# Performance work log

Hardware: AMD Instinct MI355X
Metric: run time of the kernel (lower is better)

Reference implementation:

```python
import jax, jax.numpy as jnp
import numpy as np

H = 16      # num_attention_heads
D = 1024    # hidden_size
HD = D // H # head dim = 64
ALPHA = 0.5


def setup_inputs() -> dict:
    key = jax.random.key(0)
    ks = jax.random.split(key, 12)
    B, S = 4, 1024
    s = 0.02
    return {
        "hidden_states": jax.random.normal(ks[0], (B, S, D), jnp.float32),
        "attention_mask": jnp.zeros((B, 1, 1, S), jnp.float32),
        "previous_attention": jax.random.uniform(ks[1], (B, H, S, S), jnp.float32),
        "Wq": jax.random.normal(ks[2], (D, D), jnp.float32) * s,
        "bq": jnp.zeros((D,), jnp.float32),
        "Wk": jax.random.normal(ks[3], (D, D), jnp.float32) * s,
        "bk": jnp.zeros((D,), jnp.float32),
        "Wv": jax.random.normal(ks[4], (D, D), jnp.float32) * s,
        "bv": jnp.zeros((D,), jnp.float32),
        "Wc": jax.random.normal(ks[5], (H, H), jnp.float32) * 0.25,  # 1x1 conv head-mix weight
        "bc": jnp.zeros((H,), jnp.float32),
    }


def reference(hidden_states, attention_mask, previous_attention,
              Wq, bq, Wk, bk, Wv, bv, Wc, bc):
    B, S, _ = hidden_states.shape

    def heads(x):  # [B,S,D] -> [B,H,S,HD]
        return x.reshape(B, S, H, HD).transpose(0, 2, 1, 3)

    q = heads(hidden_states @ Wq.T + bq)
    k = heads(hidden_states @ Wk.T + bk)
    v = heads(hidden_states @ Wv.T + bv)

    scores = jnp.einsum("bhsd,bhtd->bhst", q, k) / np.sqrt(HD).astype(np.float32)
    scores = scores + attention_mask
    probs = jax.nn.softmax(scores, axis=-1)

    # 1x1 conv across head channels == head-mixing matmul, then blend + re-softmax
    mixed_prev = jnp.einsum("gh,bhst->bgst", Wc, previous_attention) + bc[None, :, None, None]
    probs = jax.nn.softmax(ALPHA * mixed_prev + (1.0 - ALPHA) * probs, axis=-1)
    # dropout p=0.0 -> identity (inference)

    ctx = jnp.einsum("bhst,bhtd->bhsd", probs, v)
    ctx = ctx.transpose(0, 2, 1, 3).reshape(B, S, D)
    return ctx
```

## Files before the change

kernel.cpp:

```cpp
#include <hip/hip_runtime.h>
#include <hip/hip_bf16.h>

typedef unsigned short u16;
typedef unsigned long long u64;
typedef __attribute__((ext_vector_type(8))) short  bf16x8;
typedef __attribute__((ext_vector_type(4))) float  f32x4;
typedef __attribute__((ext_vector_type(4))) int    i32x4;
typedef __attribute__((ext_vector_type(4))) float  f32x4v;

#define MFMA16(a,b,c) __builtin_amdgcn_mfma_f32_16x16x32_bf16((a),(b),(c),0,0,0)
#define EXP2(x) __builtin_amdgcn_exp2f(x)


static constexpr size_t OFF_HBF = 0;
static constexpr size_t OFF_WBF = 8388608;
static constexpr size_t OFF_QKV = 14680064;
static constexpr size_t OFF_VT  = 31457280;
static constexpr size_t OFF_MIX = 39845888;

static constexpr float LOG2E  = 1.44269504088896340736f;
static constexpr float SSCALE = 0.125f * LOG2E;
static constexpr float HALF2E = 0.5f * LOG2E;

__device__ __forceinline__ u16 f2b(float f) {
  unsigned int u = __builtin_bit_cast(unsigned int, f);
  unsigned int r = (u + 0x7fffu + ((u >> 16) & 1u)) >> 16;
  return (u16)r;
}
__device__ __forceinline__ float b2f(u16 x) {
  union { unsigned int u; float f; } c; c.u = ((unsigned int)x) << 16; return c.f;
}

__device__ __forceinline__ void gload_lds16(const u16* g, u16* l) {
  __builtin_amdgcn_global_load_lds(
      (const __attribute__((address_space(1))) unsigned int*)g,
      (__attribute__((address_space(3))) unsigned int*)l, 16, 0, 0);
}

__global__ void __launch_bounds__(256) k_convert(
    const float* __restrict__ hid, const float* __restrict__ wq,
    const float* __restrict__ wk,  const float* __restrict__ wv,
    u16* __restrict__ hbf, u16* __restrict__ wbf)
{
  int i4 = blockIdx.x * 256 + threadIdx.x;
  f32x4v v; u16* dst;
  if (i4 < 1048576) {
    v = *(const f32x4v*)(hid + (size_t)i4 * 4);
    dst = hbf + (size_t)i4 * 4;
  } else {
    int j = (i4 - 1048576) * 4;
    const float* s = (j < 1048576) ? (wq + j)
                   : (j < 2097152) ? (wk + (j - 1048576))
                                   : (wv + (j - 2097152));
    v = *(const f32x4v*)s;
    dst = wbf + j;
  }
  u16 o[4];
  for (int k = 0; k < 4; ++k) o[k] = f2b(v[k]);
  *(u64*)dst = *(u64*)o;
}

__global__ void __launch_bounds__(256) k_qkv(
    const u16* __restrict__ Abf, const u16* __restrict__ Wbf,
    const float* __restrict__ bq, const float* __restrict__ bk,
    const float* __restrict__ bv, u16* __restrict__ qkv, u16* __restrict__ vt)
{
  __shared__ __align__(16) u16 As[2][128][32];
  __shared__ __align__(16) u16 Bs[2][128][32];
  const int n0 = blockIdx.x * 128;
  const int m0 = blockIdx.y * 128;
  const int tid = threadIdx.x;
  const int l = tid & 63, w = tid >> 6;
  const int lr = l & 15, lg = l >> 4;
  const int wm = (w >> 1) * 64, wn = (w & 1) * 64;
  const int sx = (lg ^ ((lr >> 1) & 3)) * 8;

  f32x4 acc[4][4] = {};

  auto issue = [&](int buf, int k0) {
#pragma unroll
    for (int i = 0; i < 2; ++i) {
      int c = tid + i * 256;
      int row = c >> 2, cc = c & 3;
      int gc = cc ^ ((row >> 1) & 3);
      gload_lds16(Abf + (size_t)(m0 + row) * 1024 + k0 + gc * 8, &As[buf][row][cc * 8]);
      gload_lds16(Wbf + (size_t)(n0 + row) * 1024 + k0 + gc * 8, &Bs[buf][row][cc * 8]);
    }
  };

  issue(0, 0);
  for (int k0 = 0; k0 < 1024; k0 += 32) {
    int kb = (k0 >> 5) & 1;
    __syncthreads();
    if (k0 + 32 < 1024) issue(kb ^ 1, k0 + 32);
    bf16x8 a[4], bb[4];
#pragma unroll
    for (int mi = 0; mi < 4; ++mi)
      a[mi] = *(const bf16x8*)(&As[kb][wm + mi * 16 + lr][sx]);
#pragma unroll
    for (int ni = 0; ni < 4; ++ni)
      bb[ni] = *(const bf16x8*)(&Bs[kb][wn + ni * 16 + lr][sx]);
#pragma unroll
    for (int mi = 0; mi < 4; ++mi)
#pragma unroll
      for (int ni = 0; ni < 4; ++ni)
        acc[mi][ni] = MFMA16(a[mi], bb[ni], acc[mi][ni]);
  }
#pragma unroll
  for (int mi = 0; mi < 4; ++mi)
#pragma unroll
    for (int ni = 0; ni < 4; ++ni) {
      int col = n0 + wn + ni * 16 + lr;
      const float* bias = (col < 1024) ? bq : (col < 2048) ? bk : bv;
      float bvv = bias[col & 1023];
      int rowb = m0 + wm + mi * 16 + lg * 4;
      if (col < 2048) {
#pragma unroll
        for (int r = 0; r < 4; ++r)
          qkv[(size_t)(rowb + r) * 2048 + col] = f2b(acc[mi][ni][r] + bvv);
      } else {
        int hh = (col >> 6) & 15, d = col & 63;
        int bb2 = rowb >> 10, sl = rowb & 1023;
        u16 o[4];
#pragma unroll
        for (int r = 0; r < 4; ++r) o[r] = f2b(acc[mi][ni][r] + bvv);
        *(u64*)(vt + ((size_t)(bb2 * 16 + hh) * 64 + d) * 1024 + sl) = *(u64*)o;
      }
    }
}

__global__ void __launch_bounds__(256) k_mix(
    const float* __restrict__ prev, const float* __restrict__ Wc,
    const float* __restrict__ bc, u16* __restrict__ mixed)
{
  __shared__ float wcs[256];
  __shared__ float bcs[16];
  int bsi = blockIdx.x;
  int b = bsi >> 10, s = bsi & 1023;
  int tid = threadIdx.x;
  wcs[tid] = HALF2E * Wc[tid];
  if (tid < 16) bcs[tid] = HALF2E * bc[tid];
  __syncthreads();
  size_t base = (size_t)b * 16777216 + (size_t)s * 1024;
  int t = tid * 4;
  f32x4v p[16];
#pragma unroll
  for (int hh = 0; hh < 16; ++hh)
    p[hh] = *(const f32x4v*)(prev + base + (size_t)hh * 1048576 + t);
#pragma unroll
  for (int g = 0; g < 16; ++g) {
    float bg = bcs[g];
    f32x4v a = {bg, bg, bg, bg};
#pragma unroll
    for (int hh = 0; hh < 16; ++hh)
      a += p[hh] * wcs[g * 16 + hh];
    u16 o[4];
#pragma unroll
    for (int j = 0; j < 4; ++j) o[j] = f2b(a[j]);
    *(u64*)(mixed + base + (size_t)g * 1048576 + t) = *(u64*)o;
  }
}

__global__ void __launch_bounds__(256) k_attn(
    const u16* __restrict__ qkv, const u16* __restrict__ vt,
    const u16* __restrict__ mixed, const float* __restrict__ mask,
    float* __restrict__ out)
{
  __shared__ __align__(16) char smraw[32768];
  u16   (*sc)[1024]   = (u16 (*)[1024])smraw;
  float (*ctxw)[16][64] = (float (*)[16][64])smraw;
  __shared__ float lw[4][16], l1inv[16];

  int blk = blockIdx.x;
  int sb = blk & 63, bh = blk >> 6;
  int h = bh & 15, b = bh >> 4;
  int s0 = sb * 16;
  int tid = threadIdx.x;
  int l = tid & 63, w = tid >> 6;
  int lr = l & 15, lg = l >> 4;

  const size_t qrow = (size_t)(b * 1024 + s0 + lr) * 2048 + h * 64;
  bf16x8 aq0 = *(const bf16x8*)(qkv + qrow + lg * 8);
  bf16x8 aq1 = *(const bf16x8*)(qkv + qrow + 32 + lg * 8);

#pragma unroll
  for (int tf = 0; tf < 16; ++tf) {
    int trow = w * 256 + tf * 16 + lr;
    const size_t krow = (size_t)(b * 1024 + trow) * 2048 + 1024 + h * 64;
    bf16x8 bk0 = *(const bf16x8*)(qkv + krow + lg * 8);
    bf16x8 bk1 = *(const bf16x8*)(qkv + krow + 32 + lg * 8);
    f32x4 acc = {0.f, 0.f, 0.f, 0.f};
    acc = MFMA16(aq0, bk0, acc);
    acc = MFMA16(aq1, bk1, acc);
    float mk = mask[b * 1024 + trow] * LOG2E;
#pragma unroll
    for (int r = 0; r < 4; ++r) {
      int row = lg * 4 + r;
      float sv = acc[r] * SSCALE + mk;
      int addr = (((trow >> 3) ^ (row & 7)) << 3) + (trow & 7);
      sc[row][addr] = f2b(sv);
    }
  }
  __syncthreads();

  {
    int row = tid >> 4, ch = tid & 15;
    float sm = 0.f;
#pragma unroll
    for (int c8 = 0; c8 < 8; ++c8) {
      int chunk = ch * 8 + c8;
      bf16x8 v = *(const bf16x8*)(&sc[row][(chunk ^ (row & 7)) << 3]);
#pragma unroll
      for (int j = 0; j < 8; ++j) sm += EXP2(b2f((u16)v[j]));
    }
    for (int d = 8; d >= 1; d >>= 1) sm += __shfl_xor(sm, d);
    if (ch == 0) l1inv[row] = 1.0f / sm;
  }
  __syncthreads();

  float l1h = HALF2E * l1inv[lr];
  float l2 = 0.f;
  f32x4 cacc[4] = {};
  const size_t mixrow = ((size_t)(b * 16 + h) * 1024 + s0 + lr) * 1024;
  const size_t vbase = (size_t)(b * 16 + h) * 64 * 1024;
  i32x4 mxa[8];
#pragma unroll
  for (int tt = 0; tt < 8; ++tt)
    mxa[tt] = *(const i32x4*)(mixed + mixrow + w * 256 + tt * 32 + lg * 8);
#pragma unroll
  for (int tt = 0; tt < 8; ++tt) {
    int tb = w * 256 + tt * 32 + lg * 8;
    bf16x8 s8 = *(const bf16x8*)(&sc[lr][((tb >> 3) ^ (lr & 7)) << 3]);
    const u16* mxp = (const u16*)&mxa[tt];
    bf16x8 pa;
    float ps = 0.f;
#pragma unroll
    for (int j = 0; j < 8; ++j) {
      float bl = b2f(mxp[j]) + EXP2(b2f((u16)s8[j])) * l1h;
      float p = EXP2(bl);
      ps += p;
      pa[j] = (short)f2b(p);
    }
    l2 += ps;
#pragma unroll
    for (int df = 0; df < 4; ++df) {
      bf16x8 vb = *(const bf16x8*)(vt + vbase + (size_t)(df * 16 + lr) * 1024 + tb);
      cacc[df] = MFMA16(pa, vb, cacc[df]);
    }
  }
  l2 += __shfl_xor(l2, 16);
  l2 += __shfl_xor(l2, 32);

  __syncthreads();
  if (lg == 0) lw[w][lr] = l2;
#pragma unroll
  for (int df = 0; df < 4; ++df)
#pragma unroll
    for (int r = 0; r < 4; ++r)
      ctxw[w][lg * 4 + r][df * 16 + lr] = cacc[df][r];
  __syncthreads();

  {
    int row = tid >> 4, d4 = (tid & 15) * 4;
    float den = lw[0][row] + lw[1][row] + lw[2][row] + lw[3][row];
    float inv = 1.0f / den;
    f32x4 o;
#pragma unroll
    for (int dd = 0; dd < 4; ++dd) {
      float a = ctxw[0][row][d4 + dd] + ctxw[1][row][d4 + dd] +
                ctxw[2][row][d4 + dd] + ctxw[3][row][d4 + dd];
      o[dd] = a * inv;
    }
    *(f32x4*)(out + ((size_t)(b * 1024 + s0 + row)) * 1024 + h * 64 + d4) = o;
  }
}

extern "C" void kernel_launch(void* const* d_in, const int* in_sizes, int n_in,
                              void* d_out, int out_size, void* d_ws, size_t ws_size,
                              hipStream_t stream) {
  const float* hidden = (const float*)d_in[0];
  const float* mask   = (const float*)d_in[1];
  const float* prev   = (const float*)d_in[2];
  const float* Wq     = (const float*)d_in[3];
  const float* bq     = (const float*)d_in[4];
  const float* Wk     = (const float*)d_in[5];
  const float* bk     = (const float*)d_in[6];
  const float* Wv     = (const float*)d_in[7];
  const float* bv     = (const float*)d_in[8];
  const float* Wc     = (const float*)d_in[9];
  const float* bc     = (const float*)d_in[10];
  float* out = (float*)d_out;
  char* ws = (char*)d_ws;

  u16* hbf   = (u16*)(ws + OFF_HBF);
  u16* wbf   = (u16*)(ws + OFF_WBF);
  u16* qkv   = (u16*)(ws + OFF_QKV);
  u16* vt    = (u16*)(ws + OFF_VT);
  u16* mixed = (u16*)(ws + OFF_MIX);

  k_convert<<<7168, 256, 0, stream>>>(hidden, Wq, Wk, Wv, hbf, wbf);
  k_qkv<<<dim3(24, 32), 256, 0, stream>>>(hbf, wbf, bq, bk, bv, qkv, vt);
  k_mix<<<4096, 256, 0, stream>>>(prev, Wc, bc, mixed);
  k_attn<<<4096, 256, 0, stream>>>(qkv, vt, mixed, mask, out);
}
```

Baseline: 597.7 us.

## Keep attention probabilities in registers and use 16x16x16 MFMA for PV

Restructures the attention kernel to compute S^T (K as the A operand), exponentiate in place and keep the first-softmax probabilities in registers as bf16x4, instead of staging scores through a 32KB LDS buffer and recomputing exp in a separate row-sum pass. The PV product switches to a 16x16x16 bf16 MFMA, which lets the register-resident probabilities serve directly as an operand without any LDS round trip. LDS use drops to a padded ctx reduction buffer, and launch bounds request 4 blocks per SM. The trade-off is twice as many, smaller MFMA issues and narrower global loads for V and mixed, plus an inline-asm fallback with manual nops.

```diff
diff --git a/kernel.cpp b/kernel.cpp
--- a/kernel.cpp
+++ b/kernel.cpp
@@ -4,12 +4,19 @@
 typedef unsigned short u16;
 typedef unsigned long long u64;
 typedef __attribute__((ext_vector_type(8))) short  bf16x8;
+typedef __attribute__((ext_vector_type(4))) short  bf16x4;
 typedef __attribute__((ext_vector_type(4))) float  f32x4;
 typedef __attribute__((ext_vector_type(4))) int    i32x4;
 typedef __attribute__((ext_vector_type(4))) float  f32x4v;
 
 #define MFMA16(a,b,c) __builtin_amdgcn_mfma_f32_16x16x32_bf16((a),(b),(c),0,0,0)
 #define EXP2(x) __builtin_amdgcn_exp2f(x)
+
+#if defined(__has_builtin)
+#if __has_builtin(__builtin_amdgcn_mfma_f32_16x16x16bf16_1k)
+#define HAVE_MFMA_16X16X16_BF16 1
+#endif
+#endif
 
 
 static constexpr size_t OFF_HBF = 0;
@@ -35,6 +42,16 @@
   __builtin_amdgcn_global_load_lds(
       (const __attribute__((address_space(1))) unsigned int*)g,
       (__attribute__((address_space(3))) unsigned int*)l, 16, 0, 0);
+}
+
+__device__ __forceinline__ f32x4 pv_mfma(bf16x4 a, bf16x4 b, f32x4 c) {
+#ifdef HAVE_MFMA_16X16X16_BF16
+  return __builtin_amdgcn_mfma_f32_16x16x16bf16_1k(a, b, c, 0, 0, 0);
+#else
+  asm("s_nop 1\n\tv_mfma_f32_16x16x16_bf16 %0, %1, %2, %0"
+      : "+v"(c) : "v"(a), "v"(b));
+  return c;
+#endif
 }
 
 __global__ void __launch_bounds__(256) k_convert(
@@ -161,15 +178,13 @@
   }
 }
 
-__global__ void __launch_bounds__(256) k_attn(
+__global__ void __launch_bounds__(256, 4) k_attn(
     const u16* __restrict__ qkv, const u16* __restrict__ vt,
     const u16* __restrict__ mixed, const float* __restrict__ mask,
     float* __restrict__ out)
 {
-  __shared__ __align__(16) char smraw[32768];
-  u16   (*sc)[1024]   = (u16 (*)[1024])smraw;
-  float (*ctxw)[16][64] = (float (*)[16][64])smraw;
-  __shared__ float lw[4][16], l1inv[16];
+  __shared__ float ctxw[4][16][68];
+  __shared__ float lw1[4][16], lw2[4][16];
 
   int blk = blockIdx.x;
   int sb = blk & 63, bh = blk >> 6;
@@ -177,100 +192,83 @@
   int s0 = sb * 16;
   int tid = threadIdx.x;
   int l = tid & 63, w = tid >> 6;
-  int lr = l & 15, lg = l >> 4;
-
-  const size_t qrow = (size_t)(b * 1024 + s0 + lr) * 2048 + h * 64;
-  bf16x8 aq0 = *(const bf16x8*)(qkv + qrow + lg * 8);
-  bf16x8 aq1 = *(const bf16x8*)(qkv + qrow + 32 + lg * 8);
-
-#pragma unroll
-  for (int tf = 0; tf < 16; ++tf) {
-    int trow = w * 256 + tf * 16 + lr;
-    const size_t krow = (size_t)(b * 1024 + trow) * 2048 + 1024 + h * 64;
-    bf16x8 bk0 = *(const bf16x8*)(qkv + krow + lg * 8);
-    bf16x8 bk1 = *(const bf16x8*)(qkv + krow + 32 + lg * 8);
+  int ls = l & 15, lg = l >> 4;
+  const int tw = w * 256;
+
+  const size_t qrow = (size_t)(b * 1024 + s0 + ls) * 2048 + h * 64;
+  bf16x8 bq0 = *(const bf16x8*)(qkv + qrow + lg * 8);
+  bf16x8 bq1 = *(const bf16x8*)(qkv + qrow + 32 + lg * 8);
+
+  const size_t kbase = (size_t)b * 1024 * 2048 + 1024 + h * 64;
+
+  float sum1 = 0.f;
+  bf16x4 pst[16];
+#pragma unroll
+  for (int it = 0; it < 16; ++it) {
+    int t0 = tw + it * 16;
+    const u16* kr = qkv + kbase + (size_t)(t0 + ls) * 2048;
+    bf16x8 ak0 = *(const bf16x8*)(kr + lg * 8);
+    bf16x8 ak1 = *(const bf16x8*)(kr + 32 + lg * 8);
     f32x4 acc = {0.f, 0.f, 0.f, 0.f};
-    acc = MFMA16(aq0, bk0, acc);
-    acc = MFMA16(aq1, bk1, acc);
-    float mk = mask[b * 1024 + trow] * LOG2E;
+    acc = MFMA16(ak0, bq0, acc);
+    acc = MFMA16(ak1, bq1, acc);
+    f32x4v mk4 = *(const f32x4v*)(mask + b * 1024 + t0 + lg * 4);
 #pragma unroll
     for (int r = 0; r < 4; ++r) {
-      int row = lg * 4 + r;
-      float sv = acc[r] * SSCALE + mk;
-      int addr = (((trow >> 3) ^ (row & 7)) << 3) + (trow & 7);
-      sc[row][addr] = f2b(sv);
-    }
-  }
+      float p = EXP2(acc[r] * SSCALE + mk4[r] * LOG2E);
+      sum1 += p;
+      pst[it][r] = (short)f2b(p);
+    }
+  }
+  sum1 += __shfl_xor(sum1, 16);
+  sum1 += __shfl_xor(sum1, 32);
+  if (lg == 0) lw1[w][ls] = sum1;
   __syncthreads();
-
-  {
-    int row = tid >> 4, ch = tid & 15;
-    float sm = 0.f;
-#pragma unroll
-    for (int c8 = 0; c8 < 8; ++c8) {
-      int chunk = ch * 8 + c8;
-      bf16x8 v = *(const bf16x8*)(&sc[row][(chunk ^ (row & 7)) << 3]);
-#pragma unroll
-      for (int j = 0; j < 8; ++j) sm += EXP2(b2f((u16)v[j]));
-    }
-    for (int d = 8; d >= 1; d >>= 1) sm += __shfl_xor(sm, d);
-    if (ch == 0) l1inv[row] = 1.0f / sm;
-  }
-  __syncthreads();
-
-  float l1h = HALF2E * l1inv[lr];
-  float l2 = 0.f;
+  float l1h = HALF2E / (lw1[0][ls] + lw1[1][ls] + lw1[2][ls] + lw1[3][ls]);
+
+  float den = 0.f;
   f32x4 cacc[4] = {};
-  const size_t mixrow = ((size_t)(b * 16 + h) * 1024 + s0 + lr) * 1024;
-  const size_t vbase = (size_t)(b * 16 + h) * 64 * 1024;
-  i32x4 mxa[8];
-#pragma unroll
-  for (int tt = 0; tt < 8; ++tt)
-    mxa[tt] = *(const i32x4*)(mixed + mixrow + w * 256 + tt * 32 + lg * 8);
-#pragma unroll
-  for (int tt = 0; tt < 8; ++tt) {
-    int tb = w * 256 + tt * 32 + lg * 8;
-    bf16x8 s8 = *(const bf16x8*)(&sc[lr][((tb >> 3) ^ (lr & 7)) << 3]);
-    const u16* mxp = (const u16*)&mxa[tt];
-    bf16x8 pa;
-    float ps = 0.f;
-#pragma unroll
-    for (int j = 0; j < 8; ++j) {
-      float bl = b2f(mxp[j]) + EXP2(b2f((u16)s8[j])) * l1h;
+  const size_t mixrow = ((size_t)(b * 16 + h) * 1024 + s0 + ls) * 1024;
+  const size_t vbase = (size_t)(b * 16 + h) * 65536;
+#pragma unroll
+  for (int it = 0; it < 16; ++it) {
+    int t0 = tw + it * 16;
+    u64 mxw = *(const u64*)(mixed + mixrow + t0 + lg * 4);
+    const u16* mxp = (const u16*)&mxw;
+    bf16x4 pa;
+#pragma unroll
+    for (int r = 0; r < 4; ++r) {
+      float bl = fmaf(b2f((u16)pst[it][r]), l1h, b2f(mxp[r]));
       float p = EXP2(bl);
-      ps += p;
-      pa[j] = (short)f2b(p);
-    }
-    l2 += ps;
-#pragma unroll
-    for (int df = 0; df < 4; ++df) {
-      bf16x8 vb = *(const bf16x8*)(vt + vbase + (size_t)(df * 16 + lr) * 1024 + tb);
-      cacc[df] = MFMA16(pa, vb, cacc[df]);
-    }
-  }
-  l2 += __shfl_xor(l2, 16);
-  l2 += __shfl_xor(l2, 32);
-
-  __syncthreads();
-  if (lg == 0) lw[w][lr] = l2;
-#pragma unroll
-  for (int df = 0; df < 4; ++df)
-#pragma unroll
-    for (int r = 0; r < 4; ++r)
-      ctxw[w][lg * 4 + r][df * 16 + lr] = cacc[df][r];
+      den += p;
+      pa[r] = (short)f2b(p);
+    }
+#pragma unroll
+    for (int j = 0; j < 4; ++j) {
+      bf16x4 va = *(const bf16x4*)(vt + vbase +
+                    (size_t)(j * 16 + ls) * 1024 + t0 + lg * 4);
+      cacc[j] = pv_mfma(va, pa, cacc[j]);
+    }
+  }
+  den += __shfl_xor(den, 16);
+  den += __shfl_xor(den, 32);
+#ifndef HAVE_MFMA_16X16X16_BF16
+  asm volatile("s_nop 7\n\ts_nop 7\n\ts_nop 7");
+#endif
+  if (lg == 0) lw2[w][ls] = den;
+#pragma unroll
+  for (int j = 0; j < 4; ++j)
+    *(f32x4*)(&ctxw[w][ls][j * 16 + lg * 4]) = cacc[j];
   __syncthreads();
 
   {
     int row = tid >> 4, d4 = (tid & 15) * 4;
-    float den = lw[0][row] + lw[1][row] + lw[2][row] + lw[3][row];
-    float inv = 1.0f / den;
-    f32x4 o;
-#pragma unroll
-    for (int dd = 0; dd < 4; ++dd) {
-      float a = ctxw[0][row][d4 + dd] + ctxw[1][row][d4 + dd] +
-                ctxw[2][row][d4 + dd] + ctxw[3][row][d4 + dd];
-      o[dd] = a * inv;
-    }
+    float inv = 1.0f / (lw2[0][row] + lw2[1][row] + lw2[2][row] + lw2[3][row]);
+    f32x4 a0 = *(const f32x4*)(&ctxw[0][row][d4]);
+    f32x4 a1 = *(const f32x4*)(&ctxw[1][row][d4]);
+    f32x4 a2 = *(const f32x4*)(&ctxw[2][row][d4]);
+    f32x4 a3 = *(const f32x4*)(&ctxw[3][row][d4]);
+    f32x4 o = (a0 + a1 + a2 + a3) * inv;
     *(f32x4*)(out + ((size_t)(b * 1024 + s0 + row)) * 1024 + h * 64 + d4) = o;
   }
 }
```

New measurement: 670.9 us. +12.3%, slower.
